# Performance work log

Hardware: AMD Instinct MI355X
Metric: run time of the kernel (lower is better)

Reference implementation:

```python
import jax, jax.numpy as jnp
import numpy as np

N = 65536          # particles
E = 524288         # relations (avg degree 8)
RIG = 4096         # rigid instance = particles [0, RIG); fluid = [RIG, N)
PSTEPS = 2
ATTR, STATE, RELD, NF = 3, 6, 1, 128
DT = 1.0 / 60.0
MEAN_P = np.zeros(3, np.float32); STD_P = np.ones(3, np.float32)
MEAN_V = np.zeros(3, np.float32); STD_V = np.ones(3, np.float32)


def _lin(x, w, b):
    return x @ w.T + b  # torch Linear convention: w is [out, in]


def setup_inputs() -> dict:
    key = jax.random.key(0)
    ks = iter(jax.random.split(key, 40))
    d = {}
    d["state"] = jax.random.normal(next(ks), (N, STATE), jnp.float32)
    d["attr"] = jax.random.normal(next(ks), (N, ATTR), jnp.float32)
    d["Ra"] = jax.random.normal(next(ks), (E, RELD), jnp.float32)
    d["rel_recv"] = jax.random.randint(next(ks), (E,), 0, N, jnp.int32)
    d["rel_send"] = jax.random.randint(next(ks), (E,), 0, N, jnp.int32)

    def w(shape):
        return jax.random.normal(next(ks), shape, jnp.float32) / np.sqrt(shape[1])

    d["pe_w0"] = w((NF, ATTR + 2 * STATE)); d["pe_b0"] = jnp.zeros(NF)
    d["pe_w1"] = w((NF, NF)); d["pe_b1"] = jnp.zeros(NF)
    d["re_w0"] = w((NF, 2 * ATTR + 4 * STATE + RELD)); d["re_b0"] = jnp.zeros(NF)
    d["re_w1"] = w((NF, NF)); d["re_b1"] = jnp.zeros(NF)
    d["re_w2"] = w((NF, NF)); d["re_b2"] = jnp.zeros(NF)
    d["rp_w"] = w((NF, 3 * NF)); d["rp_b"] = jnp.zeros(NF)
    d["pp_w"] = w((NF, 2 * NF)); d["pp_b"] = jnp.zeros(NF)
    d["rg_w0"] = w((NF, NF)); d["rg_b0"] = jnp.zeros(NF)
    d["rg_w1"] = w((NF, NF)); d["rg_b1"] = jnp.zeros(NF)
    d["rg_w2"] = w((7, NF)); d["rg_b2"] = jnp.zeros(7)
    d["fl_w0"] = w((NF, NF)); d["fl_b0"] = jnp.zeros(NF)
    d["fl_w1"] = w((NF, NF)); d["fl_b1"] = jnp.zeros(NF)
    d["fl_w2"] = w((3, NF)); d["fl_b2"] = jnp.zeros(3)
    return d


def reference(state, attr, Ra, rel_recv, rel_send,
              pe_w0, pe_b0, pe_w1, pe_b1,
              re_w0, re_b0, re_w1, re_b1, re_w2, re_b2,
              rp_w, rp_b, pp_w, pp_b,
              rg_w0, rg_b0, rg_w1, rg_b1, rg_w2, rg_b2,
              fl_w0, fl_b0, fl_w1, fl_b1, fl_w2, fl_b2):
    relu = jax.nn.relu
    mean_p = jnp.asarray(MEAN_P); std_p = jnp.asarray(STD_P)
    mean_v = jnp.asarray(MEAN_V); std_v = jnp.asarray(STD_V)

    # rigid-body offset (state minus instance centroid for the rigid instance)
    offset = jnp.zeros_like(state).at[:RIG].set(
        state[:RIG] - jnp.mean(state[:RIG], axis=0))
    attr2 = jnp.concatenate([attr, offset], axis=1)        # [N, ATTR+STATE]

    # f_O^enc: particle encoder on [attr2, state]
    pe_in = jnp.concatenate([attr2, state], axis=1)         # [N, 15]
    particle_encode = relu(_lin(relu(_lin(pe_in, pe_w0, pe_b0)), pe_w1, pe_b1))

    # f_R^enc: relation encoder on gathered receiver/sender features
    rel_in = jnp.concatenate([attr2[rel_recv], attr2[rel_send],
                              state[rel_recv], state[rel_send], Ra], axis=1)  # [E, 31]
    h = relu(_lin(rel_in, re_w0, re_b0))
    h = relu(_lin(h, re_w1, re_b1))
    relation_encode = relu(_lin(h, re_w2, re_b2))           # [E, NF]

    # propagation: gather effects -> f_R -> scatter-add -> f_O
    effect = jnp.zeros((N, NF), state.dtype)
    for _ in range(PSTEPS):
        r_eff = effect[rel_recv]                            # [E, NF]
        s_eff = effect[rel_send]                            # [E, NF]
        rel_eff = relu(_lin(jnp.concatenate(
            [relation_encode, r_eff, s_eff], axis=1), rp_w, rp_b))
        agg = jax.ops.segment_sum(rel_eff, rel_recv, num_segments=N)  # Rr @ rel_eff
        effect = relu(_lin(jnp.concatenate(
            [particle_encode, agg], axis=1), pp_w, pp_b))   # residual=False

    # rigid predictor: quaternion + translation of the rigid body
    pooled = jnp.mean(effect[:RIG], axis=0)                 # [NF]
    t = _lin(relu(_lin(relu(_lin(pooled, rg_w0, rg_b0)), rg_w1, rg_b1)), rg_w2, rg_b2)
    q = t[:4] / jnp.linalg.norm(t[:4])
    w, x, y, z = q[0], q[1], q[2], q[3]
    R = jnp.stack([
        jnp.stack([1.0 - 2 * (y * y + z * z), 2 * (x * y + z * w), 2 * (x * z - y * w)]),
        jnp.stack([2 * (x * y - z * w), 1.0 - 2 * (x * x + z * z), 2 * (y * z + x * w)]),
        jnp.stack([2 * (x * z + y * w), 2 * (y * z - x * w), 1.0 - 2 * (x * x + y * y)]),
    ])
    b = t[4:] * std_p
    p0 = state[:RIG, :3] * std_p + mean_p
    c = jnp.mean(p0, axis=0)
    p1 = (p0 - c) @ R + b + c
    v = (p1 - p0) / DT
    pred_rigid = (v - mean_v) / std_v                       # [RIG, 3]

    # fluid predictor: per-particle MLP
    f = relu(_lin(effect[RIG:], fl_w0, fl_b0))
    f = relu(_lin(f, fl_w1, fl_b1))
    pred_fluid = _lin(f, fl_w2, fl_b2)                      # [N-RIG, 3]

    return jnp.concatenate([pred_rigid, pred_fluid], axis=0)  # [N, 3]
```

## Files before the change

kernel.cpp:

```cpp
#include <hip/hip_runtime.h>
#include <hip/hip_bf16.h>
#include <cstdio>

#define N_P   65536
#define N_E   524288
#define RIG_  4096

typedef __attribute__((ext_vector_type(8))) short bf16x8;
typedef __attribute__((ext_vector_type(4))) float f32x4;
typedef unsigned short u16;
typedef unsigned int   u32;

__device__ __forceinline__ u16 f2b(float x) {
    __hip_bfloat16 h = __float2bfloat16(x);
    return *(u16*)&h;
}
__device__ __forceinline__ float b2f(u16 u) {
    union { unsigned u; float f; } c; c.u = ((unsigned)u) << 16; return c.f;
}
__device__ __forceinline__ unsigned pk2(float x, float y) {
    return (unsigned)f2b(x) | ((unsigned)f2b(y) << 16);
}
#define MFMA(a,b,c) __builtin_amdgcn_mfma_f32_16x16x32_bf16((a),(b),(c),0,0,0)

__device__ __forceinline__ void bar_l() {
    asm volatile("s_waitcnt lgkmcnt(0)\n\ts_barrier" ::: "memory");
}

__global__ __launch_bounds__(256) void k_hist(const int* __restrict__ recv,
                                              u32* __restrict__ cnt) {
    int i = blockIdx.x * 256 + threadIdx.x;
    if (i < N_E) atomicAdd(&cnt[recv[i]], 1u);
}
__global__ __launch_bounds__(256) void k_scan1(u32* __restrict__ data,
                                               u32* __restrict__ bsum) {
    __shared__ u32 s[256];
    int t = threadIdx.x, g = blockIdx.x * 256 + t;
    u32 v = data[g];
    s[t] = v; __syncthreads();
    for (int o = 1; o < 256; o <<= 1) {
        u32 x = (t >= o) ? s[t - o] : 0u;
        __syncthreads(); s[t] += x; __syncthreads();
    }
    data[g] = s[t] - v;
    if (t == 255) bsum[blockIdx.x] = s[255];
}
__global__ __launch_bounds__(256) void k_scan2(u32* __restrict__ bsum) {
    __shared__ u32 s[256];
    int t = threadIdx.x;
    u32 v = bsum[t];
    s[t] = v; __syncthreads();
    for (int o = 1; o < 256; o <<= 1) {
        u32 x = (t >= o) ? s[t - o] : 0u;
        __syncthreads(); s[t] += x; __syncthreads();
    }
    bsum[t] = s[t] - v;
}
__global__ __launch_bounds__(256) void k_scan3(u32* __restrict__ data,
                                               const u32* __restrict__ bsum) {
    int g = blockIdx.x * 256 + threadIdx.x;
    data[g] += bsum[blockIdx.x];
}
__global__ __launch_bounds__(256) void k_scatter(const int* __restrict__ recv,
                                                 const int* __restrict__ send,
                                                 u32* __restrict__ head,
                                                 u32* __restrict__ perm,
                                                 int* __restrict__ srecv,
                                                 int* __restrict__ ssend) {
    int i = blockIdx.x * 256 + threadIdx.x;
    if (i < N_E) {
        int n = recv[i];
        u32 pos = atomicAdd(&head[n], 1u);
        perm[pos] = (u32)i;
        srecv[pos] = n;
        ssend[pos] = send[i];
    }
}

struct CvtJob { const float* src; u16* dst; int n; int mode; int bstart; };
struct CvtArgs { CvtJob j[14]; };

__global__ __launch_bounds__(256) void k_cvt_all(CvtArgs a) {
    int b = blockIdx.x;
    int ji = 0;
    #pragma unroll
    for (int k = 1; k < 14; k++) if (b >= a.j[k].bstart) ji = k;
    CvtJob jb = a.j[ji];
    int i = (b - jb.bstart) * 256 + threadIdx.x;
    if (i >= jb.n) return;
    if (jb.mode == 0) {
        jb.dst[i] = f2b(jb.src[i]);
    } else if (jb.mode == 2) {
        int r = i >> 7;
        jb.dst[i] = (r < 3) ? f2b(jb.src[i]) : 0;
    } else if (jb.mode == 3) {
        int r = i >> 7, c = i & 127;
        jb.dst[i] = f2b(jb.src[r * 384 + c]);
    } else if (jb.mode == 4) {
        int r = i >> 7, c = i & 127;
        jb.dst[i] = f2b(jb.src[r * 256 + c]);
    } else if (jb.mode == 5) {
        int r = i >> 5, c = i & 31;
        float v = 0.f;
        if (c < 9)       v = jb.src[r * 31 + c];
        else if (c < 15) v = jb.src[r * 31 + 18 + (c - 9)];
        jb.dst[i] = f2b(v);
    } else if (jb.mode == 6) {
        int r = i >> 5, c = i & 31;
        float v = 0.f;
        if (c < 9)       v = jb.src[r * 31 + 9 + c];
        else if (c < 15) v = jb.src[r * 31 + 24 + (c - 9)];
        jb.dst[i] = f2b(v);
    } else {
        int r = i >> 5, c = i & 31;
        jb.dst[i] = (c < 15) ? f2b(jb.src[r * 15 + c]) : 0;
    }
}

__global__ __launch_bounds__(256) void k_centroid(const float* __restrict__ state,
                                                  float* __restrict__ cent) {
    int d = blockIdx.x;
    __shared__ float red[256];
    float s = 0.f;
    for (int r = threadIdx.x; r < RIG_; r += 256) s += state[r * 6 + d];
    red[threadIdx.x] = s; __syncthreads();
    for (int o = 128; o > 0; o >>= 1) {
        if (threadIdx.x < o) red[threadIdx.x] += red[threadIdx.x + o];
        __syncthreads();
    }
    if (threadIdx.x == 0) cent[d] = red[0] / (float)RIG_;
}

__global__ __launch_bounds__(256) void k_particle_ext(
        const float* __restrict__ state, const float* __restrict__ attr,
        const float* __restrict__ cent,
        const u16* __restrict__ w0r, const u16* __restrict__ w0s,
        const u16* __restrict__ pew0, const float* __restrict__ pe_b0,
        const u16* __restrict__ pew1, const float* __restrict__ pe_b1,
        const u16* __restrict__ wp,
        u16* __restrict__ P, u16* __restrict__ Q, u16* __restrict__ T) {
    __shared__ float in_s[64][16];
    __shared__ u16 INF[64 * 32];
    __shared__ __align__(16) u16 BUF[64 * 128];
    __shared__ float b0_s[128], b1_s[128];
    int t = threadIdx.x;
    int base = blockIdx.x * 64;
    if (t < 128) { b0_s[t] = pe_b0[t]; b1_s[t] = pe_b1[t]; }
    for (int it = t; it < 64 * 15; it += 256) {
        int r = it / 15, c = it % 15;
        int p = base + r;
        float v;
        if (c < 3)      v = attr[p * 3 + c];
        else if (c < 9) v = (p < RIG_) ? (state[p * 6 + (c - 3)] - cent[c - 3]) : 0.0f;
        else            v = state[p * 6 + (c - 9)];
        in_s[r][c] = v;
    }
    __syncthreads();
    int wv = t >> 6, kq4 = (t >> 4) & 3, m = t & 15;
    {
        int e = wv * 16 + m;
        u16 tmp[8];
        #pragma unroll
        for (int j = 0; j < 8; j++) {
            int k = kq4 * 8 + j;
            tmp[j] = (k < 15) ? f2b(in_s[e][k]) : (u16)0;
        }
        *(uint4*)&INF[((wv * 4 + kq4) * 16 + m) * 8] = *(uint4*)tmp;
    }
    int lane = t & 63, mm = lane & 15, quad = lane >> 4;
    bf16x8 af0 = *(const bf16x8*)&INF[((wv * 4 + quad) * 16 + mm) * 8];
    {
        f32x4 acc[8] = {};
        #pragma unroll
        for (int nt = 0; nt < 8; nt++) {
            bf16x8 bf = *(const bf16x8*)(w0r + (size_t)(nt * 16 + mm) * 32 + quad * 8);
            acc[nt] = MFMA(af0, bf, acc[nt]);
        }
        #pragma unroll
        for (int nt = 0; nt < 8; nt++) {
            int col = nt * 16 + mm;
            #pragma unroll
            for (int rg = 0; rg < 4; rg++) {
                int row = wv * 16 + quad * 4 + rg;
                P[(size_t)(base + row) * 128 + col] = f2b(acc[nt][rg]);
            }
        }
    }
    {
        f32x4 acc[8] = {};
        #pragma unroll
        for (int nt = 0; nt < 8; nt++) {
            bf16x8 bf = *(const bf16x8*)(w0s + (size_t)(nt * 16 + mm) * 32 + quad * 8);
            acc[nt] = MFMA(af0, bf, acc[nt]);
        }
        #pragma unroll
        for (int nt = 0; nt < 8; nt++) {
            int col = nt * 16 + mm;
            #pragma unroll
            for (int rg = 0; rg < 4; rg++) {
                int row = wv * 16 + quad * 4 + rg;
                Q[(size_t)(base + row) * 128 + col] = f2b(acc[nt][rg]);
            }
        }
    }
    {
        f32x4 acc[8] = {};
        #pragma unroll
        for (int nt = 0; nt < 8; nt++) {
            bf16x8 bf = *(const bf16x8*)(pew0 + (size_t)(nt * 16 + mm) * 32 + quad * 8);
            acc[nt] = MFMA(af0, bf, acc[nt]);
        }
        #pragma unroll
        for (int nt = 0; nt < 8; nt++) {
            int col = nt * 16 + mm;
            #pragma unroll
            for (int rg = 0; rg < 4; rg++) {
                BUF[((wv * 16 + (col >> 3)) * 16 + quad * 4 + rg) * 8 + (col & 7)] =
                    f2b(fmaxf(acc[nt][rg] + b0_s[col], 0.f));
            }
        }
    }
    {
        f32x4 acc[8] = {};
        for (int kc = 0; kc < 4; kc++) {
            bf16x8 af = *(const bf16x8*)&BUF[((wv * 16 + kc * 4 + quad) * 16 + mm) * 8];
            #pragma unroll
            for (int nt = 0; nt < 8; nt++) {
                bf16x8 bf = *(const bf16x8*)(pew1 + (size_t)(nt * 16 + mm) * 128 + kc * 32 + quad * 8);
                acc[nt] = MFMA(af, bf, acc[nt]);
            }
        }
        #pragma unroll
        for (int nt = 0; nt < 8; nt++) {
            int col = nt * 16 + mm;
            #pragma unroll
            for (int rg = 0; rg < 4; rg++) {
                BUF[((wv * 16 + (col >> 3)) * 16 + quad * 4 + rg) * 8 + (col & 7)] =
                    f2b(fmaxf(acc[nt][rg] + b1_s[col], 0.f));
            }
        }
    }
    {
        f32x4 acc[8] = {};
        for (int kc = 0; kc < 4; kc++) {
            bf16x8 af = *(const bf16x8*)&BUF[((wv * 16 + kc * 4 + quad) * 16 + mm) * 8];
            #pragma unroll
            for (int nt = 0; nt < 8; nt++) {
                bf16x8 bf = *(const bf16x8*)(wp + (size_t)(nt * 16 + mm) * 128 + kc * 32 + quad * 8);
                acc[nt] = MFMA(af, bf, acc[nt]);
            }
        }
        #pragma unroll
        for (int nt = 0; nt < 8; nt++) {
            int col = nt * 16 + mm;
            #pragma unroll
            for (int rg = 0; rg < 4; rg++) {
                int row = wv * 16 + quad * 4 + rg;
                T[(size_t)(base + row) * 128 + col] = f2b(acc[nt][rg]);
            }
        }
    }
}

__global__ __launch_bounds__(512, 4) void k_rel(
        const u16* __restrict__ P, const u16* __restrict__ Q,
        const float* __restrict__ Ra, const u32* __restrict__ perm,
        const int* __restrict__ srecv, const int* __restrict__ ssend,
        const float* __restrict__ re_w0_raw, const float* __restrict__ b0,
        const u16* __restrict__ w1b, const float* __restrict__ b1,
        const u16* __restrict__ w2b, const float* __restrict__ b2,
        const u16* __restrict__ wreb, const float* __restrict__ rpb,
        u16* __restrict__ Z, float* __restrict__ agg) {
    __shared__ __align__(16) u16 BUFA[64 * 136];
    __shared__ __align__(16) u16 BUFB[64 * 136];
    __shared__ int rv_s[2][64];
    __shared__ float wRa_s[128], b0_s[128], rpb_s[128];
    int t = threadIdx.x;
    if (t < 128) {
        wRa_s[t] = re_w0_raw[t * 31 + 30];
        b0_s[t] = b0[t]; rpb_s[t] = rpb[t];
    }
    int w = t >> 6, lane = t & 63, mm = lane & 15, quad = lane >> 4;
    int colw = w * 16 + mm;
    bf16x8 W1f[4], W2f[4], WEf[4];
    #pragma unroll
    for (int kc = 0; kc < 4; kc++) {
        W1f[kc] = *(const bf16x8*)(w1b  + (size_t)colw * 128 + kc * 32 + quad * 8);
        W2f[kc] = *(const bf16x8*)(w2b  + (size_t)colw * 128 + kc * 32 + quad * 8);
        WEf[kc] = *(const bf16x8*)(wreb + (size_t)colw * 128 + kc * 32 + quad * 8);
    }
    float b1c = b1[colw], b2c = b2[colw];
    int es = t >> 3, cs2 = (t & 7) * 2;
    int egs = es >> 4, ms = es & 15;
    int sseg = t >> 7, cseg = t & 127;
    int zrow = t >> 3, zc0 = (t & 7) * 16;
    const long NT = N_E / 64;
    const long stride = gridDim.x;

    long tile = blockIdx.x;
    uint4 upC0, upC1, uqC0, uqC1; float raC; int rvC;
    {
        long nb = tile * 64;
        int rvp = srecv[nb + es], svp = ssend[nb + es];
        u32 pv = perm[nb + es];
        rvC = srecv[nb + (t & 63)];
        raC = Ra[pv];
        upC0 = *(const uint4*)(P + (size_t)rvp * 128 + (size_t)cs2 * 8);
        upC1 = *(const uint4*)(P + (size_t)rvp * 128 + (size_t)(cs2 + 1) * 8);
        uqC0 = *(const uint4*)(Q + (size_t)svp * 128 + (size_t)cs2 * 8);
        uqC1 = *(const uint4*)(Q + (size_t)svp * 128 + (size_t)(cs2 + 1) * 8);
    }
    __syncthreads();
    int p = 0;
    for (; tile < NT; tile += stride) {
        long base = tile * 64;
        long ntile = tile + stride;
        bool hn = ntile < NT;
        int rvpN = 0, svpN = 0, rvN = 0; u32 pvN = 0;
        if (hn) {
            long nb = ntile * 64;
            rvpN = srecv[nb + es]; svpN = ssend[nb + es];
            pvN  = perm[nb + es];  rvN  = srecv[nb + (t & 63)];
        }
        if (t < 64) rv_s[p][t] = rvC;
        {
            #pragma unroll
            for (int ci = 0; ci < 2; ci++) {
                int kq = cs2 + ci;
                uint4 up = ci ? upC1 : upC0;
                uint4 uq = ci ? uqC1 : uqC0;
                const u16* pp = (const u16*)&up; const u16* qq = (const u16*)&uq;
                u16 outv[8];
                #pragma unroll
                for (int j = 0; j < 8; j++) {
                    int c = kq * 8 + j;
                    float v = b2f(pp[j]) + b2f(qq[j]) + raC * wRa_s[c] + b0_s[c];
                    outv[j] = f2b(fmaxf(v, 0.f));
                }
                *(uint4*)&BUFA[((egs * 16 + kq) * 16 + ms) * 8] = *(uint4*)outv;
            }
        }
        bar_l();
        uint4 upN0{}, upN1{}, uqN0{}, uqN1{}; float raN = 0.f;
        if (hn) {
            raN  = Ra[pvN];
            upN0 = *(const uint4*)(P + (size_t)rvpN * 128 + (size_t)cs2 * 8);
            upN1 = *(const uint4*)(P + (size_t)rvpN * 128 + (size_t)(cs2 + 1) * 8);
            uqN0 = *(const uint4*)(Q + (size_t)svpN * 128 + (size_t)cs2 * 8);
            uqN1 = *(const uint4*)(Q + (size_t)svpN * 128 + (size_t)(cs2 + 1) * 8);
        }
        {
            f32x4 acc[4] = {};
            #pragma unroll
            for (int eg = 0; eg < 4; eg++)
                #pragma unroll
                for (int kc = 0; kc < 4; kc++) {
                    bf16x8 af = *(const bf16x8*)&BUFA[((eg * 16 + kc * 4 + quad) * 16 + mm) * 8];
                    acc[eg] = MFMA(af, W1f[kc], acc[eg]);
                }
            #pragma unroll
            for (int eg = 0; eg < 4; eg++)
                #pragma unroll
                for (int rg = 0; rg < 4; rg++)
                    BUFB[((eg * 16 + (colw >> 3)) * 16 + quad * 4 + rg) * 8 + (colw & 7)] =
                        f2b(fmaxf(acc[eg][rg] + b1c, 0.f));
        }
        bar_l();
        {
            f32x4 acc[4] = {};
            #pragma unroll
            for (int eg = 0; eg < 4; eg++)
                #pragma unroll
                for (int kc = 0; kc < 4; kc++) {
                    bf16x8 af = *(const bf16x8*)&BUFB[((eg * 16 + kc * 4 + quad) * 16 + mm) * 8];
                    acc[eg] = MFMA(af, W2f[kc], acc[eg]);
                }
            #pragma unroll
            for (int eg = 0; eg < 4; eg++)
                #pragma unroll
                for (int rg = 0; rg < 4; rg++)
                    BUFA[((eg * 16 + (colw >> 3)) * 16 + quad * 4 + rg) * 8 + (colw & 7)] =
                        f2b(fmaxf(acc[eg][rg] + b2c, 0.f));
        }
        bar_l();
        {
            f32x4 zacc[4] = {};
            #pragma unroll
            for (int eg = 0; eg < 4; eg++)
                #pragma unroll
                for (int kc = 0; kc < 4; kc++) {
                    bf16x8 af = *(const bf16x8*)&BUFA[((eg * 16 + kc * 4 + quad) * 16 + mm) * 8];
                    zacc[eg] = MFMA(af, WEf[kc], zacc[eg]);
                }
            #pragma unroll
            for (int eg = 0; eg < 4; eg++)
                #pragma unroll
                for (int rg = 0; rg < 4; rg++)
                    BUFB[(eg * 16 + quad * 4 + rg) * 136 + colw] = f2b(zacc[eg][rg]);
        }
        bar_l();
        {
            uint4 z0 = *(const uint4*)&BUFB[zrow * 136 + zc0];
            uint4 z1 = *(const uint4*)&BUFB[zrow * 136 + zc0 + 8];
            *(uint4*)&Z[(base + zrow) * 128 + zc0]     = z0;
            *(uint4*)&Z[(base + zrow) * 128 + zc0 + 8] = z1;
        }
        {
            int r0 = sseg * 16;
            int cur = rv_s[p][r0];
            float a = fmaxf(b2f(BUFB[r0 * 136 + cseg]) + rpb_s[cseg], 0.f);
            bool first = true;
            for (int rr = r0 + 1; rr < r0 + 16; rr++) {
                int n = rv_s[p][rr];
                float v = fmaxf(b2f(BUFB[rr * 136 + cseg]) + rpb_s[cseg], 0.f);
                if (n == cur) a += v;
                else {
                    if (first) atomicAdd(&agg[(size_t)cur * 128 + cseg], a);
                    else       agg[(size_t)cur * 128 + cseg] = a;
                    first = false; cur = n; a = v;
                }
            }
            atomicAdd(&agg[(size_t)cur * 128 + cseg], a);
        }
        if (hn) { upC0 = upN0; upC1 = upN1; uqC0 = uqN0; uqC1 = uqN1; raC = raN; rvC = rvN; }
        p ^= 1;
    }
}

__global__ __launch_bounds__(256) void k_node2(
        const float* __restrict__ agg, const u16* __restrict__ T,
        const u16* __restrict__ wab, const float* __restrict__ ppb,
        u16* __restrict__ effb,
        const u16* __restrict__ wrb, const u16* __restrict__ wsb,
        u16* __restrict__ U, u16* __restrict__ V) {
    __shared__ __align__(16) u16 AF[64 * 128];
    int t = threadIdx.x;
    long base = (long)blockIdx.x * 64;
    int wv = t >> 6, kq4 = (t >> 4) & 3, m = t & 15;
    {
        long node = base + wv * 16 + m;
        #pragma unroll
        for (int i = 0; i < 4; i++) {
            int kq = kq4 + 4 * i;
            const float* src = agg + node * 128 + kq * 8;
            float4 f0 = *(const float4*)src, f1 = *(const float4*)(src + 4);
            uint4 v;
            v.x = pk2(f0.x, f0.y); v.y = pk2(f0.z, f0.w);
            v.z = pk2(f1.x, f1.y); v.w = pk2(f1.z, f1.w);
            *(uint4*)&AF[((wv * 16 + kq) * 16 + m) * 8] = v;
        }
    }
    int lane = t & 63, mm = lane & 15, quad = lane >> 4;
    f32x4 acc[8] = {};
    for (int kc = 0; kc < 4; kc++) {
        bf16x8 af = *(const bf16x8*)&AF[((wv * 16 + kc * 4 + quad) * 16 + mm) * 8];
        #pragma unroll
        for (int nt = 0; nt < 8; nt++) {
            bf16x8 bf = *(const bf16x8*)(wab + (size_t)(nt * 16 + mm) * 128 + kc * 32 + quad * 8);
            acc[nt] = MFMA(af, bf, acc[nt]);
        }
    }
    #pragma unroll
    for (int nt = 0; nt < 8; nt++) {
        int col = nt * 16 + mm;
        #pragma unroll
        for (int rg = 0; rg < 4; rg++) {
            long row = base + wv * 16 + quad * 4 + rg;
            float v = acc[nt][rg] + b2f(T[row * 128 + col]) + ppb[col];
            u16 e = f2b(fmaxf(v, 0.f));
            if (effb) effb[row * 128 + col] = e;
            AF[((wv * 16 + (col >> 3)) * 16 + quad * 4 + rg) * 8 + (col & 7)] = e;
        }
    }
    {
        f32x4 au[8] = {};
        for (int kc = 0; kc < 4; kc++) {
            bf16x8 af = *(const bf16x8*)&AF[((wv * 16 + kc * 4 + quad) * 16 + mm) * 8];
            #pragma unroll
            for (int nt = 0; nt < 8; nt++) {
                bf16x8 bu = *(const bf16x8*)(wrb + (size_t)(nt * 16 + mm) * 128 + kc * 32 + quad * 8);
                au[nt] = MFMA(af, bu, au[nt]);
            }
        }
        #pragma unroll
        for (int nt = 0; nt < 8; nt++) {
            int col = nt * 16 + mm;
            #pragma unroll
            for (int rg = 0; rg < 4; rg++) {
                long row = base + wv * 16 + quad * 4 + rg;
                U[row * 128 + col] = f2b(au[nt][rg]);
            }
        }
    }
    {
        f32x4 av[8] = {};
        for (int kc = 0; kc < 4; kc++) {
            bf16x8 af = *(const bf16x8*)&AF[((wv * 16 + kc * 4 + quad) * 16 + mm) * 8];
            #pragma unroll
            for (int nt = 0; nt < 8; nt++) {
                bf16x8 bv = *(const bf16x8*)(wsb + (size_t)(nt * 16 + mm) * 128 + kc * 32 + quad * 8);
                av[nt] = MFMA(af, bv, av[nt]);
            }
        }
        #pragma unroll
        for (int nt = 0; nt < 8; nt++) {
            int col = nt * 16 + mm;
            #pragma unroll
            for (int rg = 0; rg < 4; rg++) {
                long row = base + wv * 16 + quad * 4 + rg;
                V[row * 128 + col] = f2b(av[nt][rg]);
            }
        }
    }
}

#define HPAD 136
__global__ __launch_bounds__(256) void k_node2fl(
        const float* __restrict__ agg, const u16* __restrict__ T,
        const u16* __restrict__ wab, const float* __restrict__ ppb,
        u16* __restrict__ effb,
        const u16* __restrict__ w0b, const float* __restrict__ b0,
        const u16* __restrict__ w1b, const float* __restrict__ b1,
        const u16* __restrict__ w2b, const float* __restrict__ b2,
        float* __restrict__ out) {
    __shared__ __align__(16) u16 H[64 * HPAD];
    int t = threadIdx.x;
    long base = (long)blockIdx.x * 64;
    bool fluid = (base >= RIG_);
    int wv = t >> 6, kq4 = (t >> 4) & 3, m = t & 15;
    {
        long node = base + wv * 16 + m;
        #pragma unroll
        for (int i = 0; i < 4; i++) {
            int kq = kq4 + 4 * i;
            const float* src = agg + node * 128 + kq * 8;
            float4 f0 = *(const float4*)src, f1 = *(const float4*)(src + 4);
            uint4 v;
            v.x = pk2(f0.x, f0.y); v.y = pk2(f0.z, f0.w);
            v.z = pk2(f1.x, f1.y); v.w = pk2(f1.z, f1.w);
            *(uint4*)&H[((wv * 16 + kq) * 16 + m) * 8] = v;
        }
    }
    int lane = t & 63, mm = lane & 15, quad = lane >> 4;
    f32x4 acc[8] = {};
    for (int kc = 0; kc < 4; kc++) {
        bf16x8 af = *(const bf16x8*)&H[((wv * 16 + kc * 4 + quad) * 16 + mm) * 8];
        #pragma unroll
        for (int nt = 0; nt < 8; nt++) {
            bf16x8 bf = *(const bf16x8*)(wab + (size_t)(nt * 16 + mm) * 128 + kc * 32 + quad * 8);
            acc[nt] = MFMA(af, bf, acc[nt]);
        }
    }
    if (!fluid) {
        #pragma unroll
        for (int nt = 0; nt < 8; nt++) {
            int col = nt * 16 + mm;
            #pragma unroll
            for (int rg = 0; rg < 4; rg++) {
                long row = base + wv * 16 + quad * 4 + rg;
                float v = acc[nt][rg] + b2f(T[row * 128 + col]) + ppb[col];
                effb[row * 128 + col] = f2b(fmaxf(v, 0.f));
            }
        }
        return;
    }
    __syncthreads();
    #pragma unroll
    for (int nt = 0; nt < 8; nt++) {
        int col = nt * 16 + mm;
        #pragma unroll
        for (int rg = 0; rg < 4; rg++) {
            long row = base + wv * 16 + quad * 4 + rg;
            float v = acc[nt][rg] + b2f(T[row * 128 + col]) + ppb[col];
            H[(wv * 16 + quad * 4 + rg) * HPAD + col] = f2b(fmaxf(v, 0.f));
        }
    }
    {
        f32x4 a8[8] = {};
        for (int kc = 0; kc < 4; kc++) {
            bf16x8 af = *(const bf16x8*)&H[(wv * 16 + mm) * HPAD + kc * 32 + quad * 8];
            #pragma unroll
            for (int nt = 0; nt < 8; nt++) {
                bf16x8 bf = *(const bf16x8*)(w0b + (size_t)(nt * 16 + mm) * 128 + kc * 32 + quad * 8);
                a8[nt] = MFMA(af, bf, a8[nt]);
            }
        }
        #pragma unroll
        for (int nt = 0; nt < 8; nt++) {
            int col = nt * 16 + mm;
            float bv = b0[col];
            #pragma unroll
            for (int rg = 0; rg < 4; rg++) {
                int row = wv * 16 + quad * 4 + rg;
                H[row * HPAD + col] = f2b(fmaxf(a8[nt][rg] + bv, 0.f));
            }
        }
    }
    {
        f32x4 a8[8] = {};
        for (int kc = 0; kc < 4; kc++) {
            bf16x8 af = *(const bf16x8*)&H[(wv * 16 + mm) * HPAD + kc * 32 + quad * 8];
            #pragma unroll
            for (int nt = 0; nt < 8; nt++) {
                bf16x8 bf = *(const bf16x8*)(w1b + (size_t)(nt * 16 + mm) * 128 + kc * 32 + quad * 8);
                a8[nt] = MFMA(af, bf, a8[nt]);
            }
        }
        #pragma unroll
        for (int nt = 0; nt < 8; nt++) {
            int col = nt * 16 + mm;
            float bv = b1[col];
            #pragma unroll
            for (int rg = 0; rg < 4; rg++) {
                int row = wv * 16 + quad * 4 + rg;
                H[row * HPAD + col] = f2b(fmaxf(a8[nt][rg] + bv, 0.f));
            }
        }
    }
    {
        f32x4 a1 = {};
        for (int kc = 0; kc < 4; kc++) {
            bf16x8 af = *(const bf16x8*)&H[(wv * 16 + mm) * HPAD + kc * 32 + quad * 8];
            bf16x8 bf = *(const bf16x8*)(w2b + (size_t)mm * 128 + kc * 32 + quad * 8);
            a1 = MFMA(af, bf, a1);
        }
        if (mm < 3) {
            float bv = b2[mm];
            #pragma unroll
            for (int rg = 0; rg < 4; rg++) {
                long row = base + wv * 16 + quad * 4 + rg;
                out[row * 3 + mm] = a1[rg] + bv;
            }
        }
    }
}

__global__ __launch_bounds__(256) void k_edge2(
        const u16* __restrict__ Z, const u16* __restrict__ U, const u16* __restrict__ V,
        const int* __restrict__ srecv, const int* __restrict__ ssend,
        const float* __restrict__ rpb, float* __restrict__ agg) {
    __shared__ __align__(16) u16 S16[64 * 136];
    __shared__ int rv_s[64];
    __shared__ float rpb_s[128];
    int t = threadIdx.x;
    long base = (long)blockIdx.x * 64;
    if (t < 64) rv_s[t] = srecv[base + t];
    if (t < 128) rpb_s[t] = rpb[t];
    int r = t >> 2, q = t & 3;
    int rv = srecv[base + r];
    int sv = ssend[base + r];
    long zb = (base + r) * 128;
    size_t ub = (size_t)rv * 128, vb = (size_t)sv * 128;
    bar_l();
    #pragma unroll
    for (int i = 0; i < 4; i++) {
        int c0 = q * 32 + i * 8;
        uint4 uz = *(const uint4*)(Z + zb + c0);
        uint4 uu = *(const uint4*)(U + ub + c0);
        uint4 uv = *(const uint4*)(V + vb + c0);
        const u16* zz = (const u16*)&uz; const u16* pu = (const u16*)&uu; const u16* pv = (const u16*)&uv;
        u16 o[8];
        #pragma unroll
        for (int j = 0; j < 8; j++)
            o[j] = f2b(fmaxf(b2f(zz[j]) + b2f(pu[j]) + b2f(pv[j]) + rpb_s[c0 + j], 0.f));
        *(uint4*)&S16[r * 136 + c0] = *(uint4*)o;
    }
    bar_l();
    {
        int s = t >> 7, col = t & 127;
        int r0 = s * 32;
        int cur = rv_s[r0];
        float a = b2f(S16[r0 * 136 + col]);
        bool first = true;
        for (int rr = r0 + 1; rr < r0 + 32; rr++) {
            int n = rv_s[rr];
            float v = b2f(S16[rr * 136 + col]);
            if (n == cur) a += v;
            else {
                if (first) atomicAdd(&agg[(size_t)cur * 128 + col], a);
                else       agg[(size_t)cur * 128 + col] = a;
                first = false; cur = n; a = v;
            }
        }
        atomicAdd(&agg[(size_t)cur * 128 + col], a);
    }
}

__global__ __launch_bounds__(256) void k_pool(const u16* __restrict__ effb,
                                              float* __restrict__ pooled) {
    int f = blockIdx.x;
    __shared__ float red[256];
    float s = 0.f;
    for (int r = threadIdx.x; r < RIG_; r += 256) s += b2f(effb[(size_t)r * 128 + f]);
    red[threadIdx.x] = s; __syncthreads();
    for (int o = 128; o > 0; o >>= 1) {
        if (threadIdx.x < o) red[threadIdx.x] += red[threadIdx.x + o];
        __syncthreads();
    }
    if (threadIdx.x == 0) pooled[f] = red[0] / (float)RIG_;
}

__global__ __launch_bounds__(128) void k_rigid_head(
        const float* __restrict__ pooled,
        const float* __restrict__ w0, const float* __restrict__ b0,
        const float* __restrict__ w1, const float* __restrict__ b1,
        const float* __restrict__ w2, const float* __restrict__ b2,
        float* __restrict__ rig) {
    __shared__ float pl[128], ha[128], hb[128], tv[7];
    int t = threadIdx.x;
    pl[t] = pooled[t];
    __syncthreads();
    float a = b0[t];
    for (int k = 0; k < 128; k++) a += w0[t * 128 + k] * pl[k];
    ha[t] = fmaxf(a, 0.f);
    __syncthreads();
    a = b1[t];
    for (int k = 0; k < 128; k++) a += w1[t * 128 + k] * ha[k];
    hb[t] = fmaxf(a, 0.f);
    __syncthreads();
    if (t < 7) {
        float s = b2[t];
        for (int k = 0; k < 128; k++) s += w2[t * 128 + k] * hb[k];
        tv[t] = s;
    }
    __syncthreads();
    if (t == 0) {
        float w = tv[0], x = tv[1], y = tv[2], z = tv[3];
        float n = sqrtf(w * w + x * x + y * y + z * z);
        w /= n; x /= n; y /= n; z /= n;
        rig[0] = 1.f - 2.f * (y * y + z * z); rig[1] = 2.f * (x * y + z * w); rig[2] = 2.f * (x * z - y * w);
        rig[3] = 2.f * (x * y - z * w); rig[4] = 1.f - 2.f * (x * x + z * z); rig[5] = 2.f * (y * z + x * w);
        rig[6] = 2.f * (x * z + y * w); rig[7] = 2.f * (y * z - x * w); rig[8] = 1.f - 2.f * (x * x + y * y);
        rig[9] = tv[4]; rig[10] = tv[5]; rig[11] = tv[6];
    }
}

__global__ __launch_bounds__(256) void k_rigid_out(
        const float* __restrict__ state, const float* __restrict__ cent,
        const float* __restrict__ rig, float* __restrict__ out) {
    int i = blockIdx.x * 256 + threadIdx.x;
    if (i >= RIG_) return;
    float p0[3], d[3];
    #pragma unroll
    for (int k = 0; k < 3; k++) { p0[k] = state[i * 6 + k]; d[k] = p0[k] - cent[k]; }
    #pragma unroll
    for (int j = 0; j < 3; j++) {
        float p1 = rig[0 * 3 + j] * d[0] + rig[1 * 3 + j] * d[1] + rig[2 * 3 + j] * d[2]
                 + rig[9 + j] + cent[j];
        out[i * 3 + j] = (p1 - p0[j]) * 60.0f;
    }
}

extern "C" void kernel_launch(void* const* d_in, const int* in_sizes, int n_in,
                              void* d_out, int out_size, void* d_ws, size_t ws_size,
                              hipStream_t stream) {
    const float* state = (const float*)d_in[0];
    const float* attr  = (const float*)d_in[1];
    const float* Ra    = (const float*)d_in[2];
    const int*   recv  = (const int*)d_in[3];
    const int*   send  = (const int*)d_in[4];
    const float* pe_w0 = (const float*)d_in[5];  const float* pe_b0 = (const float*)d_in[6];
    const float* pe_w1 = (const float*)d_in[7];  const float* pe_b1 = (const float*)d_in[8];
    const float* re_w0 = (const float*)d_in[9];  const float* re_b0 = (const float*)d_in[10];
    const float* re_w1 = (const float*)d_in[11]; const float* re_b1 = (const float*)d_in[12];
    const float* re_w2 = (const float*)d_in[13]; const float* re_b2 = (const float*)d_in[14];
    const float* rp_w  = (const float*)d_in[15]; const float* rp_b  = (const float*)d_in[16];
    const float* pp_w  = (const float*)d_in[17]; const float* pp_b  = (const float*)d_in[18];
    const float* rg_w0 = (const float*)d_in[19]; const float* rg_b0 = (const float*)d_in[20];
    const float* rg_w1 = (const float*)d_in[21]; const float* rg_b1 = (const float*)d_in[22];
    const float* rg_w2 = (const float*)d_in[23]; const float* rg_b2 = (const float*)d_in[24];
    const float* fl_w0 = (const float*)d_in[25]; const float* fl_b0 = (const float*)d_in[26];
    const float* fl_w1 = (const float*)d_in[27]; const float* fl_b1 = (const float*)d_in[28];
    const float* fl_w2 = (const float*)d_in[29]; const float* fl_b2 = (const float*)d_in[30];
    float* out = (float*)d_out;

    char* p = (char*)d_ws;
    auto alloc = [&](size_t bytes) { char* r = p; p += (bytes + 255) / 256 * 256; return r; };
    float* cent    = (float*)alloc(8 * 4);
    float* pooled  = (float*)alloc(128 * 4);
    float* rig     = (float*)alloc(16 * 4);
    u32*   rowhead = (u32*)alloc((size_t)N_P * 4);
    u32*   bsum    = (u32*)alloc(256 * 4);
    u32*   perm    = (u32*)alloc((size_t)N_E * 4);
    int*   srecv   = (int*)alloc((size_t)N_E * 4);
    int*   ssend   = (int*)alloc((size_t)N_E * 4);
    float* agg     = (float*)alloc((size_t)N_P * 128 * 4);
    u16*   Z       = (u16*)alloc((size_t)N_E * 128 * 2);
    u16*   effb    = (u16*)alloc((size_t)N_P * 128 * 2);
    u16*   T       = (u16*)alloc((size_t)N_P * 128 * 2);
    u16*   P       = (u16*)alloc((size_t)N_P * 128 * 2);
    u16*   Q       = (u16*)alloc((size_t)N_P * 128 * 2);
    u16*   wreb    = (u16*)alloc(128 * 128 * 2);
    u16*   wrb     = (u16*)alloc(128 * 128 * 2);
    u16*   wsb     = (u16*)alloc(128 * 128 * 2);
    u16*   wpb     = (u16*)alloc(128 * 128 * 2);
    u16*   wab     = (u16*)alloc(128 * 128 * 2);
    u16*   rw1b    = (u16*)alloc(128 * 128 * 2);
    u16*   rw2b    = (u16*)alloc(128 * 128 * 2);
    u16*   pew1b   = (u16*)alloc(128 * 128 * 2);
    u16*   flw0b   = (u16*)alloc(128 * 128 * 2);
    u16*   flw1b   = (u16*)alloc(128 * 128 * 2);
    u16*   flw2b   = (u16*)alloc(16 * 128 * 2);
    u16*   w0rb    = (u16*)alloc(128 * 32 * 2);
    u16*   w0sb    = (u16*)alloc(128 * 32 * 2);
    u16*   pew0b   = (u16*)alloc(128 * 32 * 2);
    size_t need = (size_t)(p - (char*)d_ws);
    if (ws_size < need) {
        fprintf(stderr, "kernel_launch: ws_size %zu < needed %zu\n", ws_size, need);
        return;
    }
    u16* U = P; u16* V = Q;

    hipMemsetAsync(rowhead, 0, (size_t)N_P * 4, stream);
    k_hist<<<N_E / 256, 256, 0, stream>>>(recv, rowhead);
    k_scan1<<<N_P / 256, 256, 0, stream>>>(rowhead, bsum);
    k_scan2<<<1, 256, 0, stream>>>(bsum);
    k_scan3<<<N_P / 256, 256, 0, stream>>>(rowhead, bsum);
    k_scatter<<<N_E / 256, 256, 0, stream>>>(recv, send, rowhead, perm, srecv, ssend);

    CvtArgs ca;
    int bs = 0;
    auto addjob = [&](int idx, const float* s, u16* d, int n, int mode) {
        ca.j[idx] = {s, d, n, mode, bs};
        bs += (n + 255) / 256;
    };
    addjob(0,  rp_w,        wreb,  128 * 128, 3);
    addjob(1,  rp_w + 128,  wrb,   128 * 128, 3);
    addjob(2,  rp_w + 256,  wsb,   128 * 128, 3);
    addjob(3,  pp_w,        wpb,   128 * 128, 4);
    addjob(4,  pp_w + 128,  wab,   128 * 128, 4);
    addjob(5,  re_w1,       rw1b,  128 * 128, 0);
    addjob(6,  re_w2,       rw2b,  128 * 128, 0);
    addjob(7,  pe_w1,       pew1b, 128 * 128, 0);
    addjob(8,  fl_w0,       flw0b, 128 * 128, 0);
    addjob(9,  fl_w1,       flw1b, 128 * 128, 0);
    addjob(10, fl_w2,       flw2b, 16 * 128,  2);
    addjob(11, re_w0,       w0rb,  128 * 32,  5);
    addjob(12, re_w0,       w0sb,  128 * 32,  6);
    addjob(13, pe_w0,       pew0b, 128 * 32,  7);
    k_cvt_all<<<bs, 256, 0, stream>>>(ca);

    k_centroid<<<6, 256, 0, stream>>>(state, cent);
    k_particle_ext<<<N_P / 64, 256, 0, stream>>>(state, attr, cent,
                                                 w0rb, w0sb, pew0b, pe_b0,
                                                 pew1b, pe_b1, wpb, P, Q, T);

    hipMemsetAsync(agg, 0, (size_t)N_P * 128 * 4, stream);
    k_rel<<<512, 512, 0, stream>>>(P, Q, Ra, perm, srecv, ssend,
                                   re_w0, re_b0, rw1b, re_b1, rw2b, re_b2,
                                   wreb, rp_b, Z, agg);
    k_node2<<<N_P / 64, 256, 0, stream>>>(agg, T, wab, pp_b, nullptr, wrb, wsb, U, V);

    hipMemsetAsync(agg, 0, (size_t)N_P * 128 * 4, stream);
    k_edge2<<<N_E / 64, 256, 0, stream>>>(Z, U, V, srecv, ssend, rp_b, agg);
    k_node2fl<<<N_P / 64, 256, 0, stream>>>(agg, T, wab, pp_b, effb,
                                            flw0b, fl_b0, flw1b, fl_b1,
                                            flw2b, fl_b2, out);

    k_pool<<<128, 256, 0, stream>>>(effb, pooled);
    k_rigid_head<<<1, 128, 0, stream>>>(pooled, rg_w0, rg_b0, rg_w1, rg_b1, rg_w2, rg_b2, rig);
    k_rigid_out<<<(RIG_ + 255) / 256, 256, 0, stream>>>(state, cent, rig, out);
}
```

Before: 562.5 us.

## Retile k_rel MLP so each wave computes 16 rows x 64 columns

Changes the per-wave MFMA tiling in the relation kernel: each wave now owns one 16-row tile and 64 output columns (4 n-tiles), reusing each LDS A-fragment across 4 MFMAs instead of loading 4 A-fragments per single-column-tile wave. This cuts LDS reads but quadruples the register-resident weight fragments, so launch bounds drop to 2 blocks/CU and the grid halves to 256 blocks. The cross-iteration prefetch of gathered P/Q rows and Ra is removed, so those gathers are now issued in the same iteration they are consumed, exposing their latency.

```diff
diff --git a/kernel.cpp b/kernel.cpp
--- a/kernel.cpp
+++ b/kernel.cpp
@@ -262,7 +262,7 @@
     }
 }
 
-__global__ __launch_bounds__(512, 4) void k_rel(
+__global__ __launch_bounds__(512, 2) void k_rel(
         const u16* __restrict__ P, const u16* __restrict__ Q,
         const float* __restrict__ Ra, const u32* __restrict__ perm,
         const int* __restrict__ srecv, const int* __restrict__ ssend,
@@ -281,15 +281,21 @@
         b0_s[t] = b0[t]; rpb_s[t] = rpb[t];
     }
     int w = t >> 6, lane = t & 63, mm = lane & 15, quad = lane >> 4;
-    int colw = w * 16 + mm;
-    bf16x8 W1f[4], W2f[4], WEf[4];
+    int mt = w & 3;
+    int ch = w >> 2;
+    bf16x8 W1f[4][4], W2f[4][4], WEf[4][4];
+    float b1c[4], b2c[4];
     #pragma unroll
-    for (int kc = 0; kc < 4; kc++) {
-        W1f[kc] = *(const bf16x8*)(w1b  + (size_t)colw * 128 + kc * 32 + quad * 8);
-        W2f[kc] = *(const bf16x8*)(w2b  + (size_t)colw * 128 + kc * 32 + quad * 8);
-        WEf[kc] = *(const bf16x8*)(wreb + (size_t)colw * 128 + kc * 32 + quad * 8);
-    }
-    float b1c = b1[colw], b2c = b2[colw];
+    for (int nt = 0; nt < 4; nt++) {
+        int col = ch * 64 + nt * 16 + mm;
+        #pragma unroll
+        for (int kc = 0; kc < 4; kc++) {
+            W1f[nt][kc] = *(const bf16x8*)(w1b  + (size_t)col * 128 + kc * 32 + quad * 8);
+            W2f[nt][kc] = *(const bf16x8*)(w2b  + (size_t)col * 128 + kc * 32 + quad * 8);
+            WEf[nt][kc] = *(const bf16x8*)(wreb + (size_t)col * 128 + kc * 32 + quad * 8);
+        }
+        b1c[nt] = b1[col]; b2c[nt] = b2[col];
+    }
     int es = t >> 3, cs2 = (t & 7) * 2;
     int egs = es >> 4, ms = es & 15;
     int sseg = t >> 7, cseg = t & 127;
@@ -298,17 +304,11 @@
     const long stride = gridDim.x;
 
     long tile = blockIdx.x;
-    uint4 upC0, upC1, uqC0, uqC1; float raC; int rvC;
+    int rvpC, svpC, rvC; u32 pvC;
     {
         long nb = tile * 64;
-        int rvp = srecv[nb + es], svp = ssend[nb + es];
-        u32 pv = perm[nb + es];
-        rvC = srecv[nb + (t & 63)];
-        raC = Ra[pv];
-        upC0 = *(const uint4*)(P + (size_t)rvp * 128 + (size_t)cs2 * 8);
-        upC1 = *(const uint4*)(P + (size_t)rvp * 128 + (size_t)(cs2 + 1) * 8);
-        uqC0 = *(const uint4*)(Q + (size_t)svp * 128 + (size_t)cs2 * 8);
-        uqC1 = *(const uint4*)(Q + (size_t)svp * 128 + (size_t)(cs2 + 1) * 8);
+        rvpC = srecv[nb + es]; svpC = ssend[nb + es];
+        pvC  = perm[nb + es];  rvC  = srecv[nb + (t & 63)];
     }
     __syncthreads();
     int p = 0;
@@ -324,79 +324,78 @@
         }
         if (t < 64) rv_s[p][t] = rvC;
         {
+            float ra = Ra[pvC];
             #pragma unroll
             for (int ci = 0; ci < 2; ci++) {
                 int kq = cs2 + ci;
-                uint4 up = ci ? upC1 : upC0;
-                uint4 uq = ci ? uqC1 : uqC0;
+                uint4 up = *(const uint4*)(P + (size_t)rvpC * 128 + (size_t)kq * 8);
+                uint4 uq = *(const uint4*)(Q + (size_t)svpC * 128 + (size_t)kq * 8);
                 const u16* pp = (const u16*)&up; const u16* qq = (const u16*)&uq;
                 u16 outv[8];
                 #pragma unroll
                 for (int j = 0; j < 8; j++) {
                     int c = kq * 8 + j;
-                    float v = b2f(pp[j]) + b2f(qq[j]) + raC * wRa_s[c] + b0_s[c];
+                    float v = b2f(pp[j]) + b2f(qq[j]) + ra * wRa_s[c] + b0_s[c];
                     outv[j] = f2b(fmaxf(v, 0.f));
                 }
                 *(uint4*)&BUFA[((egs * 16 + kq) * 16 + ms) * 8] = *(uint4*)outv;
             }
         }
         bar_l();
-        uint4 upN0{}, upN1{}, uqN0{}, uqN1{}; float raN = 0.f;
-        if (hn) {
-            raN  = Ra[pvN];
-            upN0 = *(const uint4*)(P + (size_t)rvpN * 128 + (size_t)cs2 * 8);
-            upN1 = *(const uint4*)(P + (size_t)rvpN * 128 + (size_t)(cs2 + 1) * 8);
-            uqN0 = *(const uint4*)(Q + (size_t)svpN * 128 + (size_t)cs2 * 8);
-            uqN1 = *(const uint4*)(Q + (size_t)svpN * 128 + (size_t)(cs2 + 1) * 8);
-        }
         {
             f32x4 acc[4] = {};
             #pragma unroll
-            for (int eg = 0; eg < 4; eg++)
+            for (int kc = 0; kc < 4; kc++) {
+                bf16x8 af = *(const bf16x8*)&BUFA[((mt * 16 + kc * 4 + quad) * 16 + mm) * 8];
                 #pragma unroll
-                for (int kc = 0; kc < 4; kc++) {
-                    bf16x8 af = *(const bf16x8*)&BUFA[((eg * 16 + kc * 4 + quad) * 16 + mm) * 8];
-                    acc[eg] = MFMA(af, W1f[kc], acc[eg]);
-                }
-            #pragma unroll
-            for (int eg = 0; eg < 4; eg++)
+                for (int nt = 0; nt < 4; nt++)
+                    acc[nt] = MFMA(af, W1f[nt][kc], acc[nt]);
+            }
+            #pragma unroll
+            for (int nt = 0; nt < 4; nt++) {
+                int col = ch * 64 + nt * 16 + mm;
                 #pragma unroll
                 for (int rg = 0; rg < 4; rg++)
-                    BUFB[((eg * 16 + (colw >> 3)) * 16 + quad * 4 + rg) * 8 + (colw & 7)] =
-                        f2b(fmaxf(acc[eg][rg] + b1c, 0.f));
+                    BUFB[((mt * 16 + (col >> 3)) * 16 + quad * 4 + rg) * 8 + (col & 7)] =
+                        f2b(fmaxf(acc[nt][rg] + b1c[nt], 0.f));
+            }
         }
         bar_l();
         {
             f32x4 acc[4] = {};
             #pragma unroll
-            for (int eg = 0; eg < 4; eg++)
+            for (int kc = 0; kc < 4; kc++) {
+                bf16x8 af = *(const bf16x8*)&BUFB[((mt * 16 + kc * 4 + quad) * 16 + mm) * 8];
                 #pragma unroll
-                for (int kc = 0; kc < 4; kc++) {
-                    bf16x8 af = *(const bf16x8*)&BUFB[((eg * 16 + kc * 4 + quad) * 16 + mm) * 8];
-                    acc[eg] = MFMA(af, W2f[kc], acc[eg]);
-                }
-            #pragma unroll
-            for (int eg = 0; eg < 4; eg++)
+                for (int nt = 0; nt < 4; nt++)
+                    acc[nt] = MFMA(af, W2f[nt][kc], acc[nt]);
+            }
+            #pragma unroll
+            for (int nt = 0; nt < 4; nt++) {
+                int col = ch * 64 + nt * 16 + mm;
                 #pragma unroll
                 for (int rg = 0; rg < 4; rg++)
-                    BUFA[((eg * 16 + (colw >> 3)) * 16 + quad * 4 + rg) * 8 + (colw & 7)] =
-                        f2b(fmaxf(acc[eg][rg] + b2c, 0.f));
+                    BUFA[((mt * 16 + (col >> 3)) * 16 + quad * 4 + rg) * 8 + (col & 7)] =
+                        f2b(fmaxf(acc[nt][rg] + b2c[nt], 0.f));
+            }
         }
         bar_l();
         {
             f32x4 zacc[4] = {};
             #pragma unroll
-            for (int eg = 0; eg < 4; eg++)
+            for (int kc = 0; kc < 4; kc++) {
+                bf16x8 af = *(const bf16x8*)&BUFA[((mt * 16 + kc * 4 + quad) * 16 + mm) * 8];
                 #pragma unroll
-                for (int kc = 0; kc < 4; kc++) {
-                    bf16x8 af = *(const bf16x8*)&BUFA[((eg * 16 + kc * 4 + quad) * 16 + mm) * 8];
-                    zacc[eg] = MFMA(af, WEf[kc], zacc[eg]);
-                }
-            #pragma unroll
-            for (int eg = 0; eg < 4; eg++)
+                for (int nt = 0; nt < 4; nt++)
+                    zacc[nt] = MFMA(af, WEf[nt][kc], zacc[nt]);
+            }
+            #pragma unroll
+            for (int nt = 0; nt < 4; nt++) {
+                int col = ch * 64 + nt * 16 + mm;
                 #pragma unroll
                 for (int rg = 0; rg < 4; rg++)
-                    BUFB[(eg * 16 + quad * 4 + rg) * 136 + colw] = f2b(zacc[eg][rg]);
+                    BUFB[(mt * 16 + quad * 4 + rg) * 136 + col] = f2b(zacc[nt][rg]);
+            }
         }
         bar_l();
         {
@@ -422,7 +421,7 @@
             }
             atomicAdd(&agg[(size_t)cur * 128 + cseg], a);
         }
-        if (hn) { upC0 = upN0; upC1 = upN1; uqC0 = uqN0; uqC1 = uqN1; raC = raN; rvC = rvN; }
+        rvpC = rvpN; svpC = svpN; pvC = pvN; rvC = rvN;
         p ^= 1;
     }
 }
@@ -846,7 +845,7 @@
                                                  pew1b, pe_b1, wpb, P, Q, T);
 
     hipMemsetAsync(agg, 0, (size_t)N_P * 128 * 4, stream);
-    k_rel<<<512, 512, 0, stream>>>(P, Q, Ra, perm, srecv, ssend,
+    k_rel<<<256, 512, 0, stream>>>(P, Q, Ra, perm, srecv, ssend,
                                    re_w0, re_b0, rw1b, re_b1, rw2b, re_b2,
                                    wreb, rp_b, Z, agg);
     k_node2<<<N_P / 64, 256, 0, stream>>>(agg, T, wab, pp_b, nullptr, wrb, wsb, U, V);
```

Result: slower. 627.4 us (+11.5%).

## Pack sorted edge arrays into int4 and fuse rigid pooling into node kernel

Applied to the files above, without the earlier changes.

The separate perm/srecv/ssend arrays become one int4 edge record per sorted edge. Each edge's receiver, sender and original index can then be fetched with a single 16-byte load in k_rel and k_edge2. The rigid-particle effect buffer and the k_pool kernel are removed. k_node2fl now column-sums its rigid tiles from shared memory and atomically adds them into a pooled sum, which k_rigid_head scales by 1/RIG. This trades a kernel launch and an effect-buffer write and read for float atomics, which make the pooled sum order-dependent, and for a wider edge record.

```diff
diff --git a/kernel.cpp b/kernel.cpp
--- a/kernel.cpp
+++ b/kernel.cpp
@@ -64,16 +64,12 @@
 __global__ __launch_bounds__(256) void k_scatter(const int* __restrict__ recv,
                                                  const int* __restrict__ send,
                                                  u32* __restrict__ head,
-                                                 u32* __restrict__ perm,
-                                                 int* __restrict__ srecv,
-                                                 int* __restrict__ ssend) {
+                                                 int4* __restrict__ edges) {
     int i = blockIdx.x * 256 + threadIdx.x;
     if (i < N_E) {
         int n = recv[i];
         u32 pos = atomicAdd(&head[n], 1u);
-        perm[pos] = (u32)i;
-        srecv[pos] = n;
-        ssend[pos] = send[i];
+        edges[pos] = make_int4(n, send[i], i, 0);
     }
 }
 
@@ -264,8 +260,7 @@
 
 __global__ __launch_bounds__(512, 4) void k_rel(
         const u16* __restrict__ P, const u16* __restrict__ Q,
-        const float* __restrict__ Ra, const u32* __restrict__ perm,
-        const int* __restrict__ srecv, const int* __restrict__ ssend,
+        const float* __restrict__ Ra, const int4* __restrict__ edges,
         const float* __restrict__ re_w0_raw, const float* __restrict__ b0,
         const u16* __restrict__ w1b, const float* __restrict__ b1,
         const u16* __restrict__ w2b, const float* __restrict__ b2,
@@ -301,14 +296,13 @@
     uint4 upC0, upC1, uqC0, uqC1; float raC; int rvC;
     {
         long nb = tile * 64;
-        int rvp = srecv[nb + es], svp = ssend[nb + es];
-        u32 pv = perm[nb + es];
-        rvC = srecv[nb + (t & 63)];
-        raC = Ra[pv];
-        upC0 = *(const uint4*)(P + (size_t)rvp * 128 + (size_t)cs2 * 8);
-        upC1 = *(const uint4*)(P + (size_t)rvp * 128 + (size_t)(cs2 + 1) * 8);
-        uqC0 = *(const uint4*)(Q + (size_t)svp * 128 + (size_t)cs2 * 8);
-        uqC1 = *(const uint4*)(Q + (size_t)svp * 128 + (size_t)(cs2 + 1) * 8);
+        int4 e = edges[nb + es];
+        rvC = edges[nb + (t & 63)].x;
+        raC = Ra[e.z];
+        upC0 = *(const uint4*)(P + (size_t)e.x * 128 + (size_t)cs2 * 8);
+        upC1 = *(const uint4*)(P + (size_t)e.x * 128 + (size_t)(cs2 + 1) * 8);
+        uqC0 = *(const uint4*)(Q + (size_t)e.y * 128 + (size_t)cs2 * 8);
+        uqC1 = *(const uint4*)(Q + (size_t)e.y * 128 + (size_t)(cs2 + 1) * 8);
     }
     __syncthreads();
     int p = 0;
@@ -316,11 +310,11 @@
         long base = tile * 64;
         long ntile = tile + stride;
         bool hn = ntile < NT;
-        int rvpN = 0, svpN = 0, rvN = 0; u32 pvN = 0;
+        int4 eN = make_int4(0, 0, 0, 0); int rvN = 0;
         if (hn) {
             long nb = ntile * 64;
-            rvpN = srecv[nb + es]; svpN = ssend[nb + es];
-            pvN  = perm[nb + es];  rvN  = srecv[nb + (t & 63)];
+            eN  = edges[nb + es];
+            rvN = edges[nb + (t & 63)].x;
         }
         if (t < 64) rv_s[p][t] = rvC;
         {
@@ -343,11 +337,11 @@
         bar_l();
         uint4 upN0{}, upN1{}, uqN0{}, uqN1{}; float raN = 0.f;
         if (hn) {
-            raN  = Ra[pvN];
-            upN0 = *(const uint4*)(P + (size_t)rvpN * 128 + (size_t)cs2 * 8);
-            upN1 = *(const uint4*)(P + (size_t)rvpN * 128 + (size_t)(cs2 + 1) * 8);
-            uqN0 = *(const uint4*)(Q + (size_t)svpN * 128 + (size_t)cs2 * 8);
-            uqN1 = *(const uint4*)(Q + (size_t)svpN * 128 + (size_t)(cs2 + 1) * 8);
+            raN  = Ra[eN.z];
+            upN0 = *(const uint4*)(P + (size_t)eN.x * 128 + (size_t)cs2 * 8);
+            upN1 = *(const uint4*)(P + (size_t)eN.x * 128 + (size_t)(cs2 + 1) * 8);
+            uqN0 = *(const uint4*)(Q + (size_t)eN.y * 128 + (size_t)cs2 * 8);
+            uqN1 = *(const uint4*)(Q + (size_t)eN.y * 128 + (size_t)(cs2 + 1) * 8);
         }
         {
             f32x4 acc[4] = {};
@@ -430,7 +424,6 @@
 __global__ __launch_bounds__(256) void k_node2(
         const float* __restrict__ agg, const u16* __restrict__ T,
         const u16* __restrict__ wab, const float* __restrict__ ppb,
-        u16* __restrict__ effb,
         const u16* __restrict__ wrb, const u16* __restrict__ wsb,
         u16* __restrict__ U, u16* __restrict__ V) {
     __shared__ __align__(16) u16 AF[64 * 128];
@@ -468,7 +461,6 @@
             long row = base + wv * 16 + quad * 4 + rg;
             float v = acc[nt][rg] + b2f(T[row * 128 + col]) + ppb[col];
             u16 e = f2b(fmaxf(v, 0.f));
-            if (effb) effb[row * 128 + col] = e;
             AF[((wv * 16 + (col >> 3)) * 16 + quad * 4 + rg) * 8 + (col & 7)] = e;
         }
     }
@@ -518,7 +510,7 @@
 __global__ __launch_bounds__(256) void k_node2fl(
         const float* __restrict__ agg, const u16* __restrict__ T,
         const u16* __restrict__ wab, const float* __restrict__ ppb,
-        u16* __restrict__ effb,
+        float* __restrict__ pooledsum,
         const u16* __restrict__ w0b, const float* __restrict__ b0,
         const u16* __restrict__ w1b, const float* __restrict__ b1,
         const u16* __restrict__ w2b, const float* __restrict__ b2,
@@ -551,19 +543,6 @@
             acc[nt] = MFMA(af, bf, acc[nt]);
         }
     }
-    if (!fluid) {
-        #pragma unroll
-        for (int nt = 0; nt < 8; nt++) {
-            int col = nt * 16 + mm;
-            #pragma unroll
-            for (int rg = 0; rg < 4; rg++) {
-                long row = base + wv * 16 + quad * 4 + rg;
-                float v = acc[nt][rg] + b2f(T[row * 128 + col]) + ppb[col];
-                effb[row * 128 + col] = f2b(fmaxf(v, 0.f));
-            }
-        }
-        return;
-    }
     __syncthreads();
     #pragma unroll
     for (int nt = 0; nt < 8; nt++) {
@@ -574,6 +553,15 @@
             float v = acc[nt][rg] + b2f(T[row * 128 + col]) + ppb[col];
             H[(wv * 16 + quad * 4 + rg) * HPAD + col] = f2b(fmaxf(v, 0.f));
         }
+    }
+    if (!fluid) {
+        bar_l();
+        int col = t & 127, half = t >> 7;
+        float s = 0.f;
+        for (int r = half * 32; r < half * 32 + 32; r++)
+            s += b2f(H[r * HPAD + col]);
+        atomicAdd(&pooledsum[col], s);
+        return;
     }
     {
         f32x4 a8[8] = {};
@@ -637,20 +625,19 @@
 
 __global__ __launch_bounds__(256) void k_edge2(
         const u16* __restrict__ Z, const u16* __restrict__ U, const u16* __restrict__ V,
-        const int* __restrict__ srecv, const int* __restrict__ ssend,
+        const int4* __restrict__ edges,
         const float* __restrict__ rpb, float* __restrict__ agg) {
     __shared__ __align__(16) u16 S16[64 * 136];
     __shared__ int rv_s[64];
     __shared__ float rpb_s[128];
     int t = threadIdx.x;
     long base = (long)blockIdx.x * 64;
-    if (t < 64) rv_s[t] = srecv[base + t];
+    if (t < 64) rv_s[t] = edges[base + t].x;
     if (t < 128) rpb_s[t] = rpb[t];
     int r = t >> 2, q = t & 3;
-    int rv = srecv[base + r];
-    int sv = ssend[base + r];
+    int4 er = edges[base + r];
     long zb = (base + r) * 128;
-    size_t ub = (size_t)rv * 128, vb = (size_t)sv * 128;
+    size_t ub = (size_t)er.x * 128, vb = (size_t)er.y * 128;
     bar_l();
     #pragma unroll
     for (int i = 0; i < 4; i++) {
@@ -686,29 +673,15 @@
     }
 }
 
-__global__ __launch_bounds__(256) void k_pool(const u16* __restrict__ effb,
-                                              float* __restrict__ pooled) {
-    int f = blockIdx.x;
-    __shared__ float red[256];
-    float s = 0.f;
-    for (int r = threadIdx.x; r < RIG_; r += 256) s += b2f(effb[(size_t)r * 128 + f]);
-    red[threadIdx.x] = s; __syncthreads();
-    for (int o = 128; o > 0; o >>= 1) {
-        if (threadIdx.x < o) red[threadIdx.x] += red[threadIdx.x + o];
-        __syncthreads();
-    }
-    if (threadIdx.x == 0) pooled[f] = red[0] / (float)RIG_;
-}
-
 __global__ __launch_bounds__(128) void k_rigid_head(
-        const float* __restrict__ pooled,
+        const float* __restrict__ pooledsum,
         const float* __restrict__ w0, const float* __restrict__ b0,
         const float* __restrict__ w1, const float* __restrict__ b1,
         const float* __restrict__ w2, const float* __restrict__ b2,
         float* __restrict__ rig) {
     __shared__ float pl[128], ha[128], hb[128], tv[7];
     int t = threadIdx.x;
-    pl[t] = pooled[t];
+    pl[t] = pooledsum[t] * (1.0f / (float)RIG_);
     __syncthreads();
     float a = b0[t];
     for (int k = 0; k < 128; k++) a += w0[t * 128 + k] * pl[k];
@@ -781,12 +754,9 @@
     float* rig     = (float*)alloc(16 * 4);
     u32*   rowhead = (u32*)alloc((size_t)N_P * 4);
     u32*   bsum    = (u32*)alloc(256 * 4);
-    u32*   perm    = (u32*)alloc((size_t)N_E * 4);
-    int*   srecv   = (int*)alloc((size_t)N_E * 4);
-    int*   ssend   = (int*)alloc((size_t)N_E * 4);
+    int4*  edges   = (int4*)alloc((size_t)N_E * 16);
     float* agg     = (float*)alloc((size_t)N_P * 128 * 4);
     u16*   Z       = (u16*)alloc((size_t)N_E * 128 * 2);
-    u16*   effb    = (u16*)alloc((size_t)N_P * 128 * 2);
     u16*   T       = (u16*)alloc((size_t)N_P * 128 * 2);
     u16*   P       = (u16*)alloc((size_t)N_P * 128 * 2);
     u16*   Q       = (u16*)alloc((size_t)N_P * 128 * 2);
@@ -816,7 +786,7 @@
     k_scan1<<<N_P / 256, 256, 0, stream>>>(rowhead, bsum);
     k_scan2<<<1, 256, 0, stream>>>(bsum);
     k_scan3<<<N_P / 256, 256, 0, stream>>>(rowhead, bsum);
-    k_scatter<<<N_E / 256, 256, 0, stream>>>(recv, send, rowhead, perm, srecv, ssend);
+    k_scatter<<<N_E / 256, 256, 0, stream>>>(recv, send, rowhead, edges);
 
     CvtArgs ca;
     int bs = 0;
@@ -846,18 +816,18 @@
                                                  pew1b, pe_b1, wpb, P, Q, T);
 
     hipMemsetAsync(agg, 0, (size_t)N_P * 128 * 4, stream);
-    k_rel<<<512, 512, 0, stream>>>(P, Q, Ra, perm, srecv, ssend,
+    k_rel<<<512, 512, 0, stream>>>(P, Q, Ra, edges,
                                    re_w0, re_b0, rw1b, re_b1, rw2b, re_b2,
                                    wreb, rp_b, Z, agg);
-    k_node2<<<N_P / 64, 256, 0, stream>>>(agg, T, wab, pp_b, nullptr, wrb, wsb, U, V);
+    k_node2<<<N_P / 64, 256, 0, stream>>>(agg, T, wab, pp_b, wrb, wsb, U, V);
 
     hipMemsetAsync(agg, 0, (size_t)N_P * 128 * 4, stream);
-    k_edge2<<<N_E / 64, 256, 0, stream>>>(Z, U, V, srecv, ssend, rp_b, agg);
-    k_node2fl<<<N_P / 64, 256, 0, stream>>>(agg, T, wab, pp_b, effb,
+    hipMemsetAsync(pooled, 0, 128 * 4, stream);
+    k_edge2<<<N_E / 64, 256, 0, stream>>>(Z, U, V, edges, rp_b, agg);
+    k_node2fl<<<N_P / 64, 256, 0, stream>>>(agg, T, wab, pp_b, pooled,
                                             flw0b, fl_b0, flw1b, fl_b1,
                                             flw2b, fl_b2, out);
 
-    k_pool<<<128, 256, 0, stream>>>(effb, pooled);
     k_rigid_head<<<1, 128, 0, stream>>>(pooled, rg_w0, rg_b0, rg_w1, rg_b1, rg_w2, rg_b2, rig);
     k_rigid_out<<<(RIG_ + 255) / 256, 256, 0, stream>>>(state, cent, rig, out);
 }
```

After: 537.7 us. 4.4% less time.
